# Performance work log

Measured on AMD Instinct MI355X. Metric: run time of the kernel, lower is better.

## Reference

```python
import jax, jax.numpy as jnp
import numpy as np

B, S, DIN, DOUT = 2, 4096, 4096, 11008

def setup_inputs() -> dict:
    key = jax.random.key(0)
    k1, k2, k3 = jax.random.split(key, 3)
    x = jax.random.normal(k1, (B, S, DIN), dtype=jnp.float32)
    # kaiming-uniform-ish full-precision weight
    bound_w = 1.0 / np.sqrt(DIN)
    weight = jax.random.uniform(k2, (DOUT, DIN), dtype=jnp.float32, minval=-bound_w, maxval=bound_w)
    bias = jax.random.uniform(k3, (DOUT,), dtype=jnp.float32, minval=-bound_w, maxval=bound_w)
    return {"x": x, "weight": weight, "bias": bias}

def reference(x, weight, bias):
    # Binarize weight to {-1, 0, +1} via sign (matches torch.sign), scale by mean |w| (detached)
    binary_w = jnp.sign(weight)                                  # [DOUT, DIN]
    scale = jax.lax.stop_gradient(jnp.mean(jnp.abs(weight)))    # scalar
    w_q = binary_w * scale
    # F.linear: x @ w_q.T + bias
    out = jnp.einsum('bsi,oi->bso', x, w_q) + bias               # [B, S, DOUT]
    return out
```

## Files before the change

kernel.cpp:

```cpp
#include <hip/hip_runtime.h>

#define MDIM 8192
#define KDIM 4096
#define NDIM 11008

#define NBLK_W 1024

typedef float f32x4 __attribute__((ext_vector_type(4)));
typedef int   i32x4 __attribute__((ext_vector_type(4)));
typedef char  c4    __attribute__((ext_vector_type(4)));

#define GAS __attribute__((address_space(1)))
#define LAS __attribute__((address_space(3)))

__global__ __launch_bounds__(256) void k_convert_w(const float* __restrict__ w,
                                                   char* __restrict__ wq,
                                                   float* __restrict__ partials) {
  const int n4 = (NDIM * KDIM) / 4;
  const int stride = gridDim.x * blockDim.x;
  float s = 0.f;
  for (int i = blockIdx.x * blockDim.x + threadIdx.x; i < n4; i += stride) {
    f32x4 v = ((const f32x4*)w)[i];
    s += fabsf(v.x) + fabsf(v.y) + fabsf(v.z) + fabsf(v.w);
    c4 q;
    q.x = v.x > 0.f ? 1 : (v.x < 0.f ? -1 : 0);
    q.y = v.y > 0.f ? 1 : (v.y < 0.f ? -1 : 0);
    q.z = v.z > 0.f ? 1 : (v.z < 0.f ? -1 : 0);
    q.w = v.w > 0.f ? 1 : (v.w < 0.f ? -1 : 0);
    ((c4*)wq)[i] = q;
  }
  #pragma unroll
  for (int off = 32; off > 0; off >>= 1) s += __shfl_down(s, off, 64);
  __shared__ float red[4];
  if ((threadIdx.x & 63) == 0) red[threadIdx.x >> 6] = s;
  __syncthreads();
  if (threadIdx.x == 0) partials[blockIdx.x] = red[0] + red[1] + red[2] + red[3];
}

__global__ __launch_bounds__(256) void k_scale(const float* __restrict__ partials,
                                               float* __restrict__ scale) {
  float s = 0.f;
  for (int i = threadIdx.x; i < NBLK_W; i += 256) s += partials[i];
  #pragma unroll
  for (int off = 32; off > 0; off >>= 1) s += __shfl_down(s, off, 64);
  __shared__ float red[4];
  if ((threadIdx.x & 63) == 0) red[threadIdx.x >> 6] = s;
  __syncthreads();
  if (threadIdx.x == 0)
    *scale = (red[0] + red[1] + red[2] + red[3]) / (float)((size_t)NDIM * KDIM);
}

__global__ __launch_bounds__(256) void k_convert_x(const float* __restrict__ x,
                                                   char* __restrict__ xq,
                                                   float* __restrict__ sx) {
  const int row = blockIdx.x;
  const float* xr = x + (size_t)row * KDIM;
  const int t = (int)threadIdx.x;
  f32x4 v[4];
  float mx = 0.f;
  #pragma unroll
  for (int j = 0; j < 4; ++j) {
    v[j] = *(const f32x4*)(xr + j * 1024 + t * 4);
    mx = fmaxf(mx, fmaxf(fmaxf(fabsf(v[j].x), fabsf(v[j].y)),
                         fmaxf(fabsf(v[j].z), fabsf(v[j].w))));
  }
  #pragma unroll
  for (int off = 32; off > 0; off >>= 1) mx = fmaxf(mx, __shfl_xor(mx, off, 64));
  __shared__ float red[4];
  __shared__ float bmax;
  if ((t & 63) == 0) red[t >> 6] = mx;
  __syncthreads();
  if (t == 0) {
    float m2 = fmaxf(fmaxf(red[0], red[1]), fmaxf(red[2], red[3]));
    m2 = fmaxf(m2, 1e-20f);
    bmax = m2;
    sx[row] = m2 * (1.f / 127.f);
  }
  __syncthreads();
  const float r = 127.f / bmax;
  #pragma unroll
  for (int j = 0; j < 4; ++j) {
    int a = __float2int_rn(v[j].x * r), b = __float2int_rn(v[j].y * r);
    int c = __float2int_rn(v[j].z * r), d = __float2int_rn(v[j].w * r);
    a = a > 127 ? 127 : (a < -127 ? -127 : a);
    b = b > 127 ? 127 : (b < -127 ? -127 : b);
    c = c > 127 ? 127 : (c < -127 ? -127 : c);
    d = d > 127 ? 127 : (d < -127 ? -127 : d);
    c4 q; q.x = (char)a; q.y = (char)b; q.z = (char)c; q.w = (char)d;
    *(c4*)(xq + (size_t)row * KDIM + j * 1024 + t * 4) = q;
  }
}


#define BAR()  __builtin_amdgcn_s_barrier()
#define SB0()  __builtin_amdgcn_sched_barrier(0)
#define PRIO1() __builtin_amdgcn_s_setprio(1)
#define PRIO0() __builtin_amdgcn_s_setprio(0)
#define VM(N)  asm volatile("s_waitcnt vmcnt(" #N ")" ::: "memory")

#define STAGE(GP, GROWB, LDSOFF, KT) do {                                             \
  const char* _s = (GP) + (size_t)((GROWB) + srow) * KDIM + (KT)*64 + scol;           \
  char* _d = lds + (LDSOFF) + tid*16;                                                 \
  __builtin_amdgcn_global_load_lds((const GAS unsigned int*)_s,                       \
                                   (LAS unsigned int*)_d, 16, 0, 0);                  \
} while (0)

#define LOAD_B2(DST, BASE, NH)                                                        \
  _Pragma("unroll") for (int ni = 0; ni < 2; ++ni)                                    \
    DST[ni] = *(const i32x4*)&lds[(BASE) + 8192 + bWOff + (NH)*2048 + ni*1024         \
                                  + rowoff + rcol];

#define LOAD_A2(DST, BASE, MH)                                                        \
  _Pragma("unroll") for (int mi = 0; mi < 2; ++mi)                                    \
    DST[mi] = *(const i32x4*)&lds[(BASE) + aWOff + (MH)*2048 + mi*1024                \
                                  + rowoff + rcol];

#define MFMA4(AF, MB, BQ, NB)                                                         \
  _Pragma("unroll") for (int mi = 0; mi < 2; ++mi)                                    \
  _Pragma("unroll") for (int ni = 0; ni < 2; ++ni)                                    \
    acc[(MB)+mi][(NB)+ni] = __builtin_amdgcn_mfma_i32_16x16x64_i8(                    \
        AF[mi], BQ[ni], acc[(MB)+mi][(NB)+ni], 0, 0, 0);

__global__ __launch_bounds__(512, 4) void k_gemm256(const char* __restrict__ A,
                                                    const char* __restrict__ B,
                                                    const float* __restrict__ bias,
                                                    const float* __restrict__ sx,
                                                    const float* __restrict__ scale_p,
                                                    float* __restrict__ C) {
  extern __shared__ char lds[];

  const int nTn = NDIM / 256;
  const int nwg = (MDIM / 128) * nTn;
  int wg = (int)blockIdx.x;
  wg = (wg & 7) * (nwg / 8) + (wg >> 3);
  const int band = wg / (nTn * 8);
  const int rem  = wg % (nTn * 8);
  const int tn   = rem >> 3;
  const int tm   = band * 8 + (rem & 7);

  const int tid  = (int)threadIdx.x;
  const int lane = tid & 63;
  const int wave = tid >> 6;
  const int wm   = wave >> 2;
  const int wn   = wave & 3;
  const int l15  = lane & 15;

  const int rowoff = l15 * 64;
  const int rcol = ((lane >> 4) << 4) ^ (((l15 >> 1) & 3) << 4);
  const int srow = tid >> 2;
  const int scol = ((tid & 3) << 4) ^ (((tid >> 3) & 3) << 4);

  const int aWOff = wm * 4096;
  const int bWOff = wn * 4096;
  const int aRow = tm * 128;
  const int bRow = tn * 256;

  i32x4 acc[4][4];
  #pragma unroll
  for (int i = 0; i < 4; ++i)
    #pragma unroll
    for (int j = 0; j < 4; ++j) acc[i][j] = i32x4{0, 0, 0, 0};

  i32x4 af[2], bq01[2], bq23[2];

  int b_c = 0, b_n = 24576, b_s = 49152;

  STAGE(A, aRow,       0,             0);
  STAGE(B, bRow,       8192,          0);
  STAGE(B, bRow + 128, 16384,         0);
  STAGE(A, aRow,       24576,         1);
  STAGE(B, bRow,       24576 + 8192,  1);
  STAGE(B, bRow + 128, 24576 + 16384, 1);
  VM(3);
  SB0();
  BAR();
  LOAD_A2(af, 0, 0); LOAD_B2(bq01, 0, 0);

  #pragma unroll 1
  for (int i = 0; i < 64; ++i) {
    const int kS = (i + 2 > 63) ? 63 : i + 2;
    PRIO1(); MFMA4(af, 0, bq01, 0); PRIO0(); SB0();
    LOAD_B2(bq23, b_c, 1);
    STAGE(A, aRow, b_s, kS);
    BAR();
    PRIO1(); MFMA4(af, 0, bq23, 2); PRIO0(); SB0();
    LOAD_A2(af, b_c, 1);
    STAGE(B, bRow, b_s + 8192, kS);
    BAR();
    PRIO1(); MFMA4(af, 2, bq01, 0); PRIO0(); SB0();
    STAGE(B, bRow + 128, b_s + 16384, kS);
    VM(3); SB0();
    BAR();
    PRIO1(); MFMA4(af, 2, bq23, 2); PRIO0(); SB0();
    LOAD_A2(af, b_n, 0); LOAD_B2(bq01, b_n, 0);
    BAR();
    const int t = b_c; b_c = b_n; b_n = b_s; b_s = t;
  }

  VM(0);

  const float sc = *scale_p;
  float bv[4];
  #pragma unroll
  for (int ni = 0; ni < 4; ++ni) bv[ni] = bias[tn * 256 + wn * 64 + ni * 16 + l15];

  #pragma unroll
  for (int mi = 0; mi < 4; ++mi) {
    #pragma unroll
    for (int r = 0; r < 4; ++r) {
      const int m = tm * 128 + wm * 64 + mi * 16 + (lane >> 4) * 4 + r;
      const float srow_scale = sc * sx[m];
      float* crow = C + (size_t)m * NDIM + tn * 256 + wn * 64;
      #pragma unroll
      for (int ni = 0; ni < 4; ++ni)
        crow[ni * 16 + l15] = srow_scale * (float)acc[mi][ni][r] + bv[ni];
    }
  }
}

extern "C" void kernel_launch(void* const* d_in, const int* in_sizes, int n_in,
                              void* d_out, int out_size, void* d_ws, size_t ws_size,
                              hipStream_t stream) {
  const float* x = (const float*)d_in[0];
  const float* w = (const float*)d_in[1];
  const float* bias = (const float*)d_in[2];
  float* out = (float*)d_out;

  char* ws = (char*)d_ws;
  const size_t XQ_BYTES = (size_t)MDIM * KDIM;
  const size_t WQ_BYTES = (size_t)NDIM * KDIM;
  char* xq = ws;
  char* wq = ws + XQ_BYTES;
  float* sx = (float*)(ws + XQ_BYTES + WQ_BYTES);
  float* partials = sx + MDIM;
  float* scale = partials + NBLK_W;

  k_convert_w<<<NBLK_W, 256, 0, stream>>>(w, wq, partials);
  k_scale<<<1, 256, 0, stream>>>(partials, scale);
  k_convert_x<<<MDIM, 256, 0, stream>>>(x, xq, sx);

  (void)hipFuncSetAttribute((const void*)k_gemm256,
                            hipFuncAttributeMaxDynamicSharedMemorySize, 73728);
  const int grid = (MDIM / 128) * (NDIM / 256);
  k_gemm256<<<grid, 512, 73728, stream>>>(xq, wq, bias, sx, scale, out);
}
```

Measured before the change: 503.1 us.

## Merge x/w conversion kernels and restructure GEMM main loop into two phases

Folds the activation and weight quantization kernels into one launch, with block ranges split between rows of x and chunks of w, so both bandwidth-bound passes run concurrently and one launch is saved. The GEMM inner loop moves from four MFMA phases with four barriers to two phases with two barriers. All three global-to-LDS stages are issued together, and the second B fragment is preloaded, which raises register use. Fewer barriers mean less synchronisation stall, but the loads interleave less finely with the MFMAs.

```diff
diff --git a/kernel.cpp b/kernel.cpp
--- a/kernel.cpp
+++ b/kernel.cpp
@@ -13,28 +13,71 @@
 #define GAS __attribute__((address_space(1)))
 #define LAS __attribute__((address_space(3)))
 
-__global__ __launch_bounds__(256) void k_convert_w(const float* __restrict__ w,
-                                                   char* __restrict__ wq,
-                                                   float* __restrict__ partials) {
-  const int n4 = (NDIM * KDIM) / 4;
-  const int stride = gridDim.x * blockDim.x;
-  float s = 0.f;
-  for (int i = blockIdx.x * blockDim.x + threadIdx.x; i < n4; i += stride) {
-    f32x4 v = ((const f32x4*)w)[i];
-    s += fabsf(v.x) + fabsf(v.y) + fabsf(v.z) + fabsf(v.w);
-    c4 q;
-    q.x = v.x > 0.f ? 1 : (v.x < 0.f ? -1 : 0);
-    q.y = v.y > 0.f ? 1 : (v.y < 0.f ? -1 : 0);
-    q.z = v.z > 0.f ? 1 : (v.z < 0.f ? -1 : 0);
-    q.w = v.w > 0.f ? 1 : (v.w < 0.f ? -1 : 0);
-    ((c4*)wq)[i] = q;
+__global__ __launch_bounds__(256) void k_convert(const float* __restrict__ x,
+                                                 char* __restrict__ xq,
+                                                 float* __restrict__ sx,
+                                                 const float* __restrict__ w,
+                                                 char* __restrict__ wq,
+                                                 float* __restrict__ partials) {
+  const int t = (int)threadIdx.x;
+  if ((int)blockIdx.x < MDIM) {
+    const int row = blockIdx.x;
+    const float* xr = x + (size_t)row * KDIM;
+    f32x4 v[4];
+    float mx = 0.f;
+    #pragma unroll
+    for (int j = 0; j < 4; ++j) {
+      v[j] = *(const f32x4*)(xr + j * 1024 + t * 4);
+      mx = fmaxf(mx, fmaxf(fmaxf(fabsf(v[j].x), fabsf(v[j].y)),
+                           fmaxf(fabsf(v[j].z), fabsf(v[j].w))));
+    }
+    #pragma unroll
+    for (int off = 32; off > 0; off >>= 1) mx = fmaxf(mx, __shfl_xor(mx, off, 64));
+    __shared__ float red[4];
+    __shared__ float bmax;
+    if ((t & 63) == 0) red[t >> 6] = mx;
+    __syncthreads();
+    if (t == 0) {
+      float m2 = fmaxf(fmaxf(red[0], red[1]), fmaxf(red[2], red[3]));
+      m2 = fmaxf(m2, 1e-20f);
+      bmax = m2;
+      sx[row] = m2 * (1.f / 127.f);
+    }
+    __syncthreads();
+    const float r = 127.f / bmax;
+    #pragma unroll
+    for (int j = 0; j < 4; ++j) {
+      int a = __float2int_rn(v[j].x * r), b = __float2int_rn(v[j].y * r);
+      int c = __float2int_rn(v[j].z * r), d = __float2int_rn(v[j].w * r);
+      a = a > 127 ? 127 : (a < -127 ? -127 : a);
+      b = b > 127 ? 127 : (b < -127 ? -127 : b);
+      c = c > 127 ? 127 : (c < -127 ? -127 : c);
+      d = d > 127 ? 127 : (d < -127 ? -127 : d);
+      c4 q; q.x = (char)a; q.y = (char)b; q.z = (char)c; q.w = (char)d;
+      *(c4*)(xq + (size_t)row * KDIM + j * 1024 + t * 4) = q;
+    }
+  } else {
+    const int vb = (int)blockIdx.x - MDIM;
+    const int n4 = (NDIM * KDIM) / 4;
+    const int stride = NBLK_W * 256;
+    float s = 0.f;
+    for (int i = vb * 256 + t; i < n4; i += stride) {
+      f32x4 v = ((const f32x4*)w)[i];
+      s += fabsf(v.x) + fabsf(v.y) + fabsf(v.z) + fabsf(v.w);
+      c4 q;
+      q.x = v.x > 0.f ? 1 : (v.x < 0.f ? -1 : 0);
+      q.y = v.y > 0.f ? 1 : (v.y < 0.f ? -1 : 0);
+      q.z = v.z > 0.f ? 1 : (v.z < 0.f ? -1 : 0);
+      q.w = v.w > 0.f ? 1 : (v.w < 0.f ? -1 : 0);
+      ((c4*)wq)[i] = q;
+    }
+    #pragma unroll
+    for (int off = 32; off > 0; off >>= 1) s += __shfl_down(s, off, 64);
+    __shared__ float redw[4];
+    if ((t & 63) == 0) redw[t >> 6] = s;
+    __syncthreads();
+    if (t == 0) partials[vb] = redw[0] + redw[1] + redw[2] + redw[3];
   }
-  #pragma unroll
-  for (int off = 32; off > 0; off >>= 1) s += __shfl_down(s, off, 64);
-  __shared__ float red[4];
-  if ((threadIdx.x & 63) == 0) red[threadIdx.x >> 6] = s;
-  __syncthreads();
-  if (threadIdx.x == 0) partials[blockIdx.x] = red[0] + red[1] + red[2] + red[3];
 }
 
 __global__ __launch_bounds__(256) void k_scale(const float* __restrict__ partials,
@@ -48,47 +91,6 @@
   __syncthreads();
   if (threadIdx.x == 0)
     *scale = (red[0] + red[1] + red[2] + red[3]) / (float)((size_t)NDIM * KDIM);
-}
-
-__global__ __launch_bounds__(256) void k_convert_x(const float* __restrict__ x,
-                                                   char* __restrict__ xq,
-                                                   float* __restrict__ sx) {
-  const int row = blockIdx.x;
-  const float* xr = x + (size_t)row * KDIM;
-  const int t = (int)threadIdx.x;
-  f32x4 v[4];
-  float mx = 0.f;
-  #pragma unroll
-  for (int j = 0; j < 4; ++j) {
-    v[j] = *(const f32x4*)(xr + j * 1024 + t * 4);
-    mx = fmaxf(mx, fmaxf(fmaxf(fabsf(v[j].x), fabsf(v[j].y)),
-                         fmaxf(fabsf(v[j].z), fabsf(v[j].w))));
-  }
-  #pragma unroll
-  for (int off = 32; off > 0; off >>= 1) mx = fmaxf(mx, __shfl_xor(mx, off, 64));
-  __shared__ float red[4];
-  __shared__ float bmax;
-  if ((t & 63) == 0) red[t >> 6] = mx;
-  __syncthreads();
-  if (t == 0) {
-    float m2 = fmaxf(fmaxf(red[0], red[1]), fmaxf(red[2], red[3]));
-    m2 = fmaxf(m2, 1e-20f);
-    bmax = m2;
-    sx[row] = m2 * (1.f / 127.f);
-  }
-  __syncthreads();
-  const float r = 127.f / bmax;
-  #pragma unroll
-  for (int j = 0; j < 4; ++j) {
-    int a = __float2int_rn(v[j].x * r), b = __float2int_rn(v[j].y * r);
-    int c = __float2int_rn(v[j].z * r), d = __float2int_rn(v[j].w * r);
-    a = a > 127 ? 127 : (a < -127 ? -127 : a);
-    b = b > 127 ? 127 : (b < -127 ? -127 : b);
-    c = c > 127 ? 127 : (c < -127 ? -127 : c);
-    d = d > 127 ? 127 : (d < -127 ? -127 : d);
-    c4 q; q.x = (char)a; q.y = (char)b; q.z = (char)c; q.w = (char)d;
-    *(c4*)(xq + (size_t)row * KDIM + j * 1024 + t * 4) = q;
-  }
 }
 
 
@@ -174,25 +176,20 @@
   VM(3);
   SB0();
   BAR();
-  LOAD_A2(af, 0, 0); LOAD_B2(bq01, 0, 0);
+  LOAD_A2(af, 0, 0); LOAD_B2(bq01, 0, 0); LOAD_B2(bq23, 0, 1);
 
   #pragma unroll 1
   for (int i = 0; i < 64; ++i) {
     const int kS = (i + 2 > 63) ? 63 : i + 2;
-    PRIO1(); MFMA4(af, 0, bq01, 0); PRIO0(); SB0();
-    LOAD_B2(bq23, b_c, 1);
-    STAGE(A, aRow, b_s, kS);
-    BAR();
-    PRIO1(); MFMA4(af, 0, bq23, 2); PRIO0(); SB0();
+    PRIO1(); MFMA4(af, 0, bq01, 0); MFMA4(af, 0, bq23, 2); PRIO0(); SB0();
     LOAD_A2(af, b_c, 1);
-    STAGE(B, bRow, b_s + 8192, kS);
-    BAR();
-    PRIO1(); MFMA4(af, 2, bq01, 0); PRIO0(); SB0();
+    STAGE(A, aRow,       b_s,         kS);
+    STAGE(B, bRow,       b_s + 8192,  kS);
     STAGE(B, bRow + 128, b_s + 16384, kS);
     VM(3); SB0();
     BAR();
-    PRIO1(); MFMA4(af, 2, bq23, 2); PRIO0(); SB0();
-    LOAD_A2(af, b_n, 0); LOAD_B2(bq01, b_n, 0);
+    PRIO1(); MFMA4(af, 2, bq01, 0); MFMA4(af, 2, bq23, 2); PRIO0(); SB0();
+    LOAD_A2(af, b_n, 0); LOAD_B2(bq01, b_n, 0); LOAD_B2(bq23, b_n, 1);
     BAR();
     const int t = b_c; b_c = b_n; b_n = b_s; b_s = t;
   }
@@ -235,9 +232,8 @@
   float* partials = sx + MDIM;
   float* scale = partials + NBLK_W;
 
-  k_convert_w<<<NBLK_W, 256, 0, stream>>>(w, wq, partials);
+  k_convert<<<MDIM + NBLK_W, 256, 0, stream>>>(x, xq, sx, w, wq, partials);
   k_scale<<<1, 256, 0, stream>>>(partials, scale);
-  k_convert_x<<<MDIM, 256, 0, stream>>>(x, xq, sx);
 
   (void)hipFuncSetAttribute((const void*)k_gemm256,
                             hipFuncAttributeMaxDynamicSharedMemorySize, 73728);
```

Result: no change. 510.0 us (+1.4%).

## Load B fragments directly from global into registers, stage only A in LDS

Applied to the files above, without the earlier changes.

The weight (B) operand now goes straight from global memory into registers, one k-step ahead, instead of being staged through LDS. Only the activation (A) tile stays triple-buffered in LDS, so dynamic LDS drops from 72KB to 24KB and the main loop has fewer barriers and MFMA phases. The aim is to cut LDS traffic and synchronization and to allow more resident workgroups. The cost is that waves sharing B columns now fetch them twice from global, the row-strided 16-byte loads coalesce worse, and global latency is hidden by only one iteration of register prefetch.

```diff
diff --git a/kernel.cpp b/kernel.cpp
--- a/kernel.cpp
+++ b/kernel.cpp
@@ -98,28 +98,30 @@
 #define PRIO0() __builtin_amdgcn_s_setprio(0)
 #define VM(N)  asm volatile("s_waitcnt vmcnt(" #N ")" ::: "memory")
 
-#define STAGE(GP, GROWB, LDSOFF, KT) do {                                             \
-  const char* _s = (GP) + (size_t)((GROWB) + srow) * KDIM + (KT)*64 + scol;           \
+#define STAGE_A(LDSOFF, KT) do {                                                      \
+  const char* _s = A + (size_t)(aRow + srow) * KDIM + (KT)*64 + scol;                 \
   char* _d = lds + (LDSOFF) + tid*16;                                                 \
   __builtin_amdgcn_global_load_lds((const GAS unsigned int*)_s,                       \
                                    (LAS unsigned int*)_d, 16, 0, 0);                  \
 } while (0)
 
-#define LOAD_B2(DST, BASE, NH)                                                        \
-  _Pragma("unroll") for (int ni = 0; ni < 2; ++ni)                                    \
-    DST[ni] = *(const i32x4*)&lds[(BASE) + 8192 + bWOff + (NH)*2048 + ni*1024         \
-                                  + rowoff + rcol];
-
 #define LOAD_A2(DST, BASE, MH)                                                        \
   _Pragma("unroll") for (int mi = 0; mi < 2; ++mi)                                    \
-    DST[mi] = *(const i32x4*)&lds[(BASE) + aWOff + (MH)*2048 + mi*1024                \
-                                  + rowoff + rcol];
+    (DST)[mi] = *(const i32x4*)&lds[(BASE) + aWOff + (MH)*2048 + mi*1024              \
+                                    + rowoff + rcol];
+
+#define LOADG_B(KT) do {                                                              \
+  _Pragma("unroll") for (int ni = 0; ni < 2; ++ni) {                                  \
+    bq01[ni] = *(const i32x4*)(bgp + (size_t)(ni * 16) * KDIM + (size_t)(KT) * 64);   \
+    bq23[ni] = *(const i32x4*)(bgp + (size_t)((ni + 2) * 16) * KDIM + (size_t)(KT) * 64); \
+  }                                                                                   \
+} while (0)
 
 #define MFMA4(AF, MB, BQ, NB)                                                         \
   _Pragma("unroll") for (int mi = 0; mi < 2; ++mi)                                    \
   _Pragma("unroll") for (int ni = 0; ni < 2; ++ni)                                    \
     acc[(MB)+mi][(NB)+ni] = __builtin_amdgcn_mfma_i32_16x16x64_i8(                    \
-        AF[mi], BQ[ni], acc[(MB)+mi][(NB)+ni], 0, 0, 0);
+        (AF)[mi], (BQ)[ni], acc[(MB)+mi][(NB)+ni], 0, 0, 0);
 
 __global__ __launch_bounds__(512, 4) void k_gemm256(const char* __restrict__ A,
                                                     const char* __restrict__ B,
@@ -151,9 +153,10 @@
   const int scol = ((tid & 3) << 4) ^ (((tid >> 3) & 3) << 4);
 
   const int aWOff = wm * 4096;
-  const int bWOff = wn * 4096;
   const int aRow = tm * 128;
   const int bRow = tn * 256;
+
+  const char* bgp = B + (size_t)(bRow + wn * 64 + l15) * KDIM + ((lane >> 4) << 4);
 
   i32x4 acc[4][4];
   #pragma unroll
@@ -161,38 +164,32 @@
     #pragma unroll
     for (int j = 0; j < 4; ++j) acc[i][j] = i32x4{0, 0, 0, 0};
 
-  i32x4 af[2], bq01[2], bq23[2];
-
-  int b_c = 0, b_n = 24576, b_s = 49152;
-
-  STAGE(A, aRow,       0,             0);
-  STAGE(B, bRow,       8192,          0);
-  STAGE(B, bRow + 128, 16384,         0);
-  STAGE(A, aRow,       24576,         1);
-  STAGE(B, bRow,       24576 + 8192,  1);
-  STAGE(B, bRow + 128, 24576 + 16384, 1);
-  VM(3);
+  i32x4 af[4], bq01[2], bq23[2];
+
+  int b_c = 0, b_n = 8192, b_s = 16384;
+
+  LOADG_B(0);
+  SB0();
+  STAGE_A(0,    0);
+  STAGE_A(8192, 1);
+  VM(1);
   SB0();
   BAR();
-  LOAD_A2(af, 0, 0); LOAD_B2(bq01, 0, 0);
+  LOAD_A2(af, 0, 0);
 
   #pragma unroll 1
   for (int i = 0; i < 64; ++i) {
+    const int kB = (i + 1 > 63) ? 63 : i + 1;
     const int kS = (i + 2 > 63) ? 63 : i + 2;
-    PRIO1(); MFMA4(af, 0, bq01, 0); PRIO0(); SB0();
-    LOAD_B2(bq23, b_c, 1);
-    STAGE(A, aRow, b_s, kS);
+    PRIO1(); MFMA4(af, 0, bq01, 0); MFMA4(af, 0, bq23, 2); PRIO0(); SB0();
+    LOAD_A2(af + 2, b_c, 1);
     BAR();
-    PRIO1(); MFMA4(af, 0, bq23, 2); PRIO0(); SB0();
-    LOAD_A2(af, b_c, 1);
-    STAGE(B, bRow, b_s + 8192, kS);
-    BAR();
-    PRIO1(); MFMA4(af, 2, bq01, 0); PRIO0(); SB0();
-    STAGE(B, bRow + 128, b_s + 16384, kS);
-    VM(3); SB0();
-    BAR();
-    PRIO1(); MFMA4(af, 2, bq23, 2); PRIO0(); SB0();
-    LOAD_A2(af, b_n, 0); LOAD_B2(bq01, b_n, 0);
+    PRIO1(); MFMA4(af + 2, 2, bq01, 0); MFMA4(af + 2, 2, bq23, 2); PRIO0(); SB0();
+    LOADG_B(kB);
+    SB0();
+    STAGE_A(b_s, kS);
+    VM(5); SB0();
+    LOAD_A2(af, b_n, 0);
     BAR();
     const int t = b_c; b_c = b_n; b_n = b_s; b_s = t;
   }
@@ -240,7 +237,7 @@
   k_convert_x<<<MDIM, 256, 0, stream>>>(x, xq, sx);
 
   (void)hipFuncSetAttribute((const void*)k_gemm256,
-                            hipFuncAttributeMaxDynamicSharedMemorySize, 73728);
+                            hipFuncAttributeMaxDynamicSharedMemorySize, 24576);
   const int grid = (MDIM / 128) * (NDIM / 256);
-  k_gemm256<<<grid, 512, 73728, stream>>>(xq, wq, bias, sx, scale, out);
-}
+  k_gemm256<<<grid, 512, 24576, stream>>>(xq, wq, bias, sx, scale, out);
+}
```

New measurement: 903.6 us. +79.6%, slower.
